# Performance work log

Hardware: AMD Instinct MI355X
Metric: run time of the kernel (lower is better)

The kernel has to match this reference:

```python
import jax, jax.numpy as jnp
import numpy as np
import itertools

F = 3          # num_sparse_features
C = 256        # num_categories
D = 64         # embedding_dim
H = 1024       # hidden_units
ND = 13        # num_dense_features
B = 16384      # batch
COMBOS = [c for r in range(2, F + 1) for c in itertools.combinations(range(F), r)]
WIDE_DIM = C * F + sum(C ** len(c) for c in COMBOS) + ND
DEEP_IN = F * D + ND


def setup_inputs() -> dict:
    key = jax.random.key(0)
    ks = jax.random.split(key, 12)
    sparse_inputs = jax.random.randint(ks[0], (B, F), 0, C, dtype=jnp.int32)
    dense_inputs = jax.random.normal(ks[1], (B, ND), dtype=jnp.float32)
    wide_w = jax.random.normal(ks[2], (WIDE_DIM,), dtype=jnp.float32) * 0.01
    wide_b = jax.random.normal(ks[3], (1,), dtype=jnp.float32) * 0.01
    emb = jax.random.normal(ks[4], (F, C, D), dtype=jnp.float32) * 0.05
    W1 = jax.random.normal(ks[5], (H, DEEP_IN), dtype=jnp.float32) / np.sqrt(DEEP_IN).astype(np.float32)
    b1 = jnp.zeros((H,), jnp.float32)
    W2 = jax.random.normal(ks[6], (H, H), dtype=jnp.float32) / np.sqrt(H).astype(np.float32)
    b2 = jnp.zeros((H,), jnp.float32)
    W3 = jax.random.normal(ks[7], (1, H), dtype=jnp.float32) / np.sqrt(H).astype(np.float32)
    b3 = jnp.zeros((1,), jnp.float32)
    return {"sparse_inputs": sparse_inputs, "dense_inputs": dense_inputs,
            "wide_w": wide_w, "wide_b": wide_b, "emb": emb,
            "W1": W1, "b1": b1, "W2": W2, "b2": b2, "W3": W3, "b3": b3}


def reference(sparse_inputs, dense_inputs, wide_w, wide_b, emb, W1, b1, W2, b2, W3, b3):
    # Wide path: one_hot(x) @ W.T  ==  gather of W columns at the hot indices.
    wide = wide_b[0]  # scalar, broadcasts to [B]
    for i in range(F):  # per-feature one-hot block, width C each
        wide = wide + wide_w[i * C + sparse_inputs[:, i]]
    off = F * C
    for combo in COMBOS:  # cross-feature one-hot blocks, width C**len(combo)
        cross = sparse_inputs[:, combo[0]]
        for j in combo[1:]:
            # faithful to source: multiplies by num_sparse_features (F), not C
            cross = cross * F + sparse_inputs[:, j]
        wide = wide + wide_w[off + cross]
        off += C ** len(combo)
    wide = wide + dense_inputs @ wide_w[off:off + ND]  # dense tail of wide linear
    wide = wide[:, None]  # [B, 1]

    # Deep path: per-feature embedding lookup -> concat -> 3-layer MLP
    embedded = jnp.concatenate([emb[i][sparse_inputs[:, i]] for i in range(F)], axis=1)  # [B, F*D]
    deep_x = jnp.concatenate([embedded, dense_inputs], axis=1)  # [B, DEEP_IN]
    h = jax.nn.relu(deep_x @ W1.T + b1)
    h = jax.nn.relu(h @ W2.T + b2)
    deep = h @ W3.T + b3  # [B, 1]

    return jax.nn.sigmoid(wide + deep)
```

## Files before the change

kernel.cpp:

```cpp
#include <hip/hip_runtime.h>
#include <stdint.h>


#define BATCH 16384
#define HDIM 1024
#define K1 224
#define DEEP_IN 205

typedef short bf16x8 __attribute__((ext_vector_type(8)));
typedef float f32x4 __attribute__((ext_vector_type(4)));
typedef uint16_t u16x8 __attribute__((ext_vector_type(8)));
typedef uint16_t u16x4 __attribute__((ext_vector_type(4)));

__device__ __forceinline__ uint16_t f2bf(float f) {
    uint32_t x;
    __builtin_memcpy(&x, &f, 4);
    uint32_t r = (x + 0x7fffu + ((x >> 16) & 1u)) >> 16;
    return (uint16_t)r;
}

__device__ __forceinline__ void async_ld16(const uint16_t* g, uint16_t* l) {
    __builtin_amdgcn_global_load_lds(
        (const __attribute__((address_space(1))) uint32_t*)g,
        (__attribute__((address_space(3))) uint32_t*)l, 16, 0, 0);
}

__global__ __launch_bounds__(256) void prep_kernel(
    const int* __restrict__ sp, const float* __restrict__ dense,
    const float* __restrict__ emb, const float* __restrict__ W1,
    uint16_t* __restrict__ dx, uint16_t* __restrict__ W1b)
{
    const int bid = blockIdx.x;
    if (bid < 1792) {
        int idx = bid * 256 + threadIdx.x;
        int b = idx / 28, c0 = (idx - b * 28) * 8;
        u16x8 o;
        if (c0 < 192) {
            int f = c0 >> 6, cc = c0 & 63;
            int s = sp[b * 3 + f];
            const float* e = emb + (size_t)(((f << 8) + s) * 64 + cc);
            float4 v0 = *(const float4*)e;
            float4 v1 = *(const float4*)(e + 4);
            o[0] = f2bf(v0.x); o[1] = f2bf(v0.y); o[2] = f2bf(v0.z); o[3] = f2bf(v0.w);
            o[4] = f2bf(v1.x); o[5] = f2bf(v1.y); o[6] = f2bf(v1.z); o[7] = f2bf(v1.w);
        } else {
#pragma unroll
            for (int t = 0; t < 8; t++) {
                int c = c0 + t;
                o[t] = (c < DEEP_IN) ? f2bf(dense[b * 13 + (c - 192)])
                                     : (uint16_t)0;
            }
        }
        *(u16x8*)(dx + (size_t)b * K1 + c0) = o;
    } else {
        int idx = (bid - 1792) * 256 + threadIdx.x;
        int n = idx / 28, c0 = (idx - n * 28) * 8;
        u16x8 o;
#pragma unroll
        for (int t = 0; t < 8; t++) {
            int c = c0 + t;
            o[t] = (c < DEEP_IN) ? f2bf(W1[n * DEEP_IN + c]) : (uint16_t)0;
        }
        *(u16x8*)(W1b + (size_t)n * K1 + c0) = o;
    }
}

#define GEMM_CORE(A_, B_, K_)                                                  \
    const int lane = tid & 63;                                                 \
    const int wave = tid >> 6;                                                 \
    const int wm = wave >> 2;                                                  \
    const int wn = wave & 3;                                                   \
    const int xcd = id & 7;                                                    \
    const int slot = id >> 3;                                                  \
    const int mbX = (M >> 7) >> 3;                                             \
    const int by = xcd * mbX + (slot >> 2);                                    \
    const int bx = slot & 3;                                                   \
    const int bm = by * 128;                                                   \
    const int bn = bx * 256;                                                   \
    const int rl = lane & 15, q = lane >> 4;                                   \
    f32x4 acc[4][4];                                                           \
    _Pragma("unroll") for (int i = 0; i < 4; i++)                              \
        _Pragma("unroll") for (int j = 0; j < 4; j++) acc[i][j] = (f32x4)0.f;  \
    const int cc0 = 2 * wave, cc1 = 2 * wave + 1;                              \
    const uint16_t* aS = A_ + (size_t)(bm + wave * 16 + rl) * K_ + q * 8;      \
    const uint16_t* bS0 = B_ + (size_t)(bn + (cc0 >> 2) * 64 + 4 * rl + (cc0 & 3)) * K_ + q * 8; \
    const uint16_t* bS1 = B_ + (size_t)(bn + (cc1 >> 2) * 64 + 4 * rl + (cc1 & 3)) * K_ + q * 8; \
    const int dA = wave * 512, dB0 = cc0 * 512, dB1 = cc1 * 512;               \
    async_ld16(aS, &Al[0][dA]);                                                \
    async_ld16(bS0, &Bl[0][dB0]);                                              \
    async_ld16(bS1, &Bl[0][dB1]);                                              \
    asm volatile("s_waitcnt vmcnt(0)" ::: "memory");                           \
    __syncthreads();                                                           \
    int p = 0;                                                                 \
    for (int k0 = 32; k0 < K_; k0 += 32) {                                     \
        async_ld16(aS + k0, &Al[p ^ 1][dA]);                                   \
        async_ld16(bS0 + k0, &Bl[p ^ 1][dB0]);                                 \
        async_ld16(bS1 + k0, &Bl[p ^ 1][dB1]);                                 \
        bf16x8 af[4], bfr[4];                                                  \
        _Pragma("unroll") for (int i = 0; i < 4; i++)                          \
            af[i] = *(const bf16x8*)&Al[p][(wm * 4 + i) * 512 + lane * 8];     \
        _Pragma("unroll") for (int j = 0; j < 4; j++)                          \
            bfr[j] = *(const bf16x8*)&Bl[p][(wn * 4 + j) * 512 + lane * 8];    \
        _Pragma("unroll") for (int i = 0; i < 4; i++)                          \
            _Pragma("unroll") for (int j = 0; j < 4; j++)                      \
                acc[i][j] = __builtin_amdgcn_mfma_f32_16x16x32_bf16(           \
                    af[i], bfr[j], acc[i][j], 0, 0, 0);                        \
        asm volatile("s_waitcnt vmcnt(0)" ::: "memory");                       \
        __syncthreads();                                                       \
        p ^= 1;                                                                \
    }                                                                          \
    {                                                                          \
        bf16x8 af[4], bfr[4];                                                  \
        _Pragma("unroll") for (int i = 0; i < 4; i++)                          \
            af[i] = *(const bf16x8*)&Al[p][(wm * 4 + i) * 512 + lane * 8];     \
        _Pragma("unroll") for (int j = 0; j < 4; j++)                          \
            bfr[j] = *(const bf16x8*)&Bl[p][(wn * 4 + j) * 512 + lane * 8];    \
        _Pragma("unroll") for (int i = 0; i < 4; i++)                          \
            _Pragma("unroll") for (int j = 0; j < 4; j++)                      \
                acc[i][j] = __builtin_amdgcn_mfma_f32_16x16x32_bf16(           \
                    af[i], bfr[j], acc[i][j], 0, 0, 0);                        \
    }

__global__ __launch_bounds__(512, 4) void gemm_relu(
    const uint16_t* __restrict__ A, const uint16_t* __restrict__ Bw,
    const float* __restrict__ bias, uint16_t* __restrict__ C,
    const float* __restrict__ W2, uint16_t* __restrict__ W2b,
    const int* __restrict__ sp, const float* __restrict__ dense,
    const float* __restrict__ ww, const float* __restrict__ wb,
    const float* __restrict__ b3, float* __restrict__ wide,
    int M, int N, int K)
{
    const int id = blockIdx.x;
    const int tid = threadIdx.x;

    if (id >= 512) {
        if (id < 768) {
            int k = (id - 512) * 512 + tid;
            const float* src = W2 + (size_t)k * 8;
            float4 v0 = *(const float4*)src;
            float4 v1 = *(const float4*)(src + 4);
            u16x8 o;
            o[0] = f2bf(v0.x); o[1] = f2bf(v0.y); o[2] = f2bf(v0.z); o[3] = f2bf(v0.w);
            o[4] = f2bf(v1.x); o[5] = f2bf(v1.y); o[6] = f2bf(v1.z); o[7] = f2bf(v1.w);
            *(u16x8*)(W2b + (size_t)k * 8) = o;
        } else {
            int b = (id - 768) * 512 + tid;
            int s0 = sp[b * 3], s1 = sp[b * 3 + 1], s2 = sp[b * 3 + 2];
            float w = wb[0] + b3[0];
            w += ww[s0] + ww[256 + s1] + ww[512 + s2];
            w += ww[768    + s0 * 3 + s1];
            w += ww[66304  + s0 * 3 + s2];
            w += ww[131840 + s1 * 3 + s2];
            w += ww[197376 + (s0 * 3 + s1) * 3 + s2];
            const float* wd = ww + 16974592;
            float acc2 = 0.f;
#pragma unroll
            for (int j = 0; j < 13; j++) acc2 += dense[b * 13 + j] * wd[j];
            wide[b] = w + acc2;
        }
        return;
    }

    __shared__ __align__(16) uint16_t Al[2][4096];
    __shared__ __align__(16) uint16_t Bl[2][8192];
    GEMM_CORE(A, Bw, K)

    float bv[4];
#pragma unroll
    for (int j = 0; j < 4; j++) bv[j] = bias[bn + wn * 64 + 4 * rl + j];
#pragma unroll
    for (int i = 0; i < 4; i++) {
#pragma unroll
        for (int r = 0; r < 4; r++) {
            int m = bm + wm * 64 + i * 16 + q * 4 + r;
            u16x4 o;
#pragma unroll
            for (int j = 0; j < 4; j++)
                o[j] = f2bf(fmaxf(acc[i][j][r] + bv[j], 0.f));
            *(u16x4*)&C[(size_t)m * N + bn + wn * 64 + 4 * rl] = o;
        }
    }
}

#define BAR8() do { asm volatile("" ::: "memory");                             \
    __builtin_amdgcn_s_barrier();                                              \
    asm volatile("" ::: "memory"); } while (0)
#define VM4() asm volatile("s_waitcnt vmcnt(4)" ::: "memory")

#define STG8(grow, regoff, h, kt) do {                                         \
    const uint16_t* g_ = (grow) + (size_t)((h) * 128) * (size_t)K + (kt);      \
    async_ld16(g_, &lds[(regoff) + (h) * 8192 + wave * 512]);                  \
    async_ld16(g_ + (size_t)64 * (size_t)K,                                    \
               &lds[(regoff) + (h) * 8192 + 4096 + wave * 512]);               \
} while (0)

#define LDA8(base, msub) do {                                                  \
    _Pragma("unroll") for (int mt = 0; mt < 4; mt++) {                         \
        int ro_ = (base) + ((msub) * 64 + mt * 16) * 64;                       \
        af[mt][0] = *(const bf16x8*)&lds[ro_ + kc0];                           \
        af[mt][1] = *(const bf16x8*)&lds[ro_ + kc1];                           \
    } } while (0)

#define LDB8(dst, base, nsub) do {                                             \
    _Pragma("unroll") for (int nt = 0; nt < 2; nt++) {                         \
        int ro_ = (base) + ((nsub) * 32 + nt * 16) * 64;                       \
        dst[nt][0] = *(const bf16x8*)&lds[ro_ + kc0];                          \
        dst[nt][1] = *(const bf16x8*)&lds[ro_ + kc1];                          \
    } } while (0)

#define MM8(msub, nsub, BF) do {                                               \
    __builtin_amdgcn_s_setprio(1);                                             \
    _Pragma("unroll") for (int mt = 0; mt < 4; mt++)                           \
    _Pragma("unroll") for (int nt = 0; nt < 2; nt++) {                         \
        acc[(msub)*4+mt][(nsub)*2+nt] = __builtin_amdgcn_mfma_f32_16x16x32_bf16( \
            af[mt][0], BF[nt][0], acc[(msub)*4+mt][(nsub)*2+nt], 0, 0, 0);     \
        acc[(msub)*4+mt][(nsub)*2+nt] = __builtin_amdgcn_mfma_f32_16x16x32_bf16( \
            af[mt][1], BF[nt][1], acc[(msub)*4+mt][(nsub)*2+nt], 0, 0, 0);     \
    }                                                                          \
    __builtin_amdgcn_s_setprio(0); } while (0)

__global__ __launch_bounds__(512, 2) void gemm_fused8(
    const uint16_t* __restrict__ A, const uint16_t* __restrict__ Bw,
    const float* __restrict__ bias, const float* __restrict__ W3,
    float* __restrict__ outacc, int M, int N, int K)
{
    __shared__ __align__(16) uint16_t lds[65536];
    const int tid = threadIdx.x;
    const int lane = tid & 63, wave = tid >> 6;
    const int wm = wave >> 2, wn = wave & 3;
    const int id = blockIdx.x;
    const int wg = (id & 7) * 32 + (id >> 3);
    const int by = wg >> 2, bx = wg & 3;
    const int bm = by * 256, bn = bx * 256;

    const int lam = lane & 15, lad = lane >> 4;
    const int sw = (lane & 7) << 4;
    const int kc0 = ((lad * 16) ^ sw) >> 1;
    const int kc1 = ((64 + lad * 16) ^ sw) >> 1;
    const int aBE = wm * 8192 + lam * 64;
    const int aBO = aBE + 16384;
    const int bBE = 32768 + (wn >> 1) * 8192 + ((wn & 1) * 64 + lam) * 64;
    const int bBO = bBE + 16384;

    const int trow = tid >> 3;
    const int csel = ((tid & 7) ^ (trow & 7)) << 3;
    const uint16_t* aRow = A + (size_t)(bm + trow) * K + csel;
    const uint16_t* bRow = Bw + (size_t)(bn + trow) * K + csel;

    f32x4 acc[8][4];
#pragma unroll
    for (int i = 0; i < 8; i++)
#pragma unroll
        for (int j = 0; j < 4; j++) acc[i][j] = (f32x4)0.f;
    bf16x8 af[4][2], bf0[2][2], bf1[2][2];

    const int NT = K >> 6;
    const int NI = K >> 7;

    STG8(aRow, 0, 0, 0);     STG8(aRow, 0, 1, 0);
    STG8(bRow, 32768, 0, 0); STG8(bRow, 32768, 1, 0);
    STG8(bRow, 49152, 0, 64); STG8(bRow, 49152, 1, 64);
    VM4();
    BAR8();

    for (int it = 0; it < NI; ++it) {
        const int k1 = (2 * it + 1) * 64;
        const int t2 = 2 * it + 2, t3 = 2 * it + 3;
        const int k2 = (t2 < NT ? t2 : 0) * 64;
        const int k3 = (t3 < NT ? t3 : 0) * 64;
        LDA8(aBE, 0); LDB8(bf0, bBE, 0); STG8(aRow, 16384, 0, k1);
        BAR8(); MM8(0, 0, bf0); BAR8();
        LDB8(bf1, bBE, 1); STG8(aRow, 16384, 1, k1);
        BAR8(); MM8(0, 1, bf1); BAR8();
        LDA8(aBE, 1); STG8(bRow, 32768, 0, k2);
        BAR8(); MM8(1, 1, bf1); BAR8();
        STG8(bRow, 32768, 1, k2);
        BAR8(); MM8(1, 0, bf0); VM4(); BAR8();
        LDA8(aBO, 0); LDB8(bf0, bBO, 0); STG8(aRow, 0, 0, k2);
        BAR8(); MM8(0, 0, bf0); BAR8();
        LDB8(bf1, bBO, 1); STG8(aRow, 0, 1, k2);
        BAR8(); MM8(0, 1, bf1); BAR8();
        LDA8(aBO, 1); STG8(bRow, 49152, 0, k3);
        BAR8(); MM8(1, 1, bf1); BAR8();
        STG8(bRow, 49152, 1, k3);
        BAR8(); MM8(1, 0, bf0); VM4(); BAR8();
    }

    float bv[4], w3v[4];
#pragma unroll
    for (int jn = 0; jn < 4; jn++) {
        int n = bn + wn * 64 + jn * 16 + lam;
        bv[jn] = bias[n];
        w3v[jn] = W3[n];
    }
#pragma unroll
    for (int im = 0; im < 8; im++) {
#pragma unroll
        for (int r = 0; r < 4; r++) {
            float pt = 0.f;
#pragma unroll
            for (int jn = 0; jn < 4; jn++)
                pt += fmaxf(acc[im][jn][r] + bv[jn], 0.f) * w3v[jn];
            pt += __shfl_xor(pt, 1);
            pt += __shfl_xor(pt, 2);
            pt += __shfl_xor(pt, 4);
            pt += __shfl_xor(pt, 8);
            if (lam == 0) {
                int m = bm + wm * 128 + im * 16 + lad * 4 + r;
                atomicAdd(&outacc[m], pt);
            }
        }
    }
}

__global__ __launch_bounds__(256) void sigmoid_kernel(
    const float* __restrict__ outacc, float* __restrict__ out)
{
    int b = blockIdx.x * 256 + threadIdx.x;
    out[b] = 1.f / (1.f + __expf(-outacc[b]));
}

extern "C" void kernel_launch(void* const* d_in, const int* in_sizes, int n_in,
                              void* d_out, int out_size, void* d_ws, size_t ws_size,
                              hipStream_t stream) {
    const int*   sp    = (const int*)d_in[0];
    const float* dense = (const float*)d_in[1];
    const float* ww    = (const float*)d_in[2];
    const float* wb    = (const float*)d_in[3];
    const float* emb   = (const float*)d_in[4];
    const float* W1    = (const float*)d_in[5];
    const float* b1    = (const float*)d_in[6];
    const float* W2    = (const float*)d_in[7];
    const float* b2    = (const float*)d_in[8];
    const float* W3    = (const float*)d_in[9];
    const float* b3    = (const float*)d_in[10];
    float* out = (float*)d_out;

    char* ws = (char*)d_ws;
    float*    wide = (float*)ws;
    uint16_t* dxp  = (uint16_t*)(ws + 65536);
    uint16_t* W1b  = (uint16_t*)(ws + 7405568);
    uint16_t* W2b  = (uint16_t*)(ws + 7864320);
    uint16_t* h1   = (uint16_t*)(ws + 9961472);

    prep_kernel<<<1904, 256, 0, stream>>>(sp, dense, emb, W1, dxp, W1b);
    gemm_relu<<<800, 512, 0, stream>>>(
        dxp, W1b, b1, h1, W2, W2b, sp, dense, ww, wb, b3, wide,
        BATCH, HDIM, K1);
    gemm_fused8<<<(BATCH / 256) * (HDIM / 256), 512, 0, stream>>>(
        h1, W2b, b2, W3, wide, BATCH, HDIM, HDIM);
    sigmoid_kernel<<<BATCH / 256, 256, 0, stream>>>(wide, out);
}
```

Baseline: 162.5 us.

## Pad layer-1 K to 256 and reuse the 256x256 pipelined GEMM for layer 1

```diff
diff --git a/kernel.cpp b/kernel.cpp
--- a/kernel.cpp
+++ b/kernel.cpp
@@ -4,7 +4,7 @@
 
 #define BATCH 16384
 #define HDIM 1024
-#define K1 224
+#define K1 256
 #define DEEP_IN 205
 
 typedef short bf16x8 __attribute__((ext_vector_type(8)));
@@ -28,12 +28,16 @@
 __global__ __launch_bounds__(256) void prep_kernel(
     const int* __restrict__ sp, const float* __restrict__ dense,
     const float* __restrict__ emb, const float* __restrict__ W1,
-    uint16_t* __restrict__ dx, uint16_t* __restrict__ W1b)
+    const float* __restrict__ W2, const float* __restrict__ ww,
+    const float* __restrict__ wb, const float* __restrict__ b3,
+    uint16_t* __restrict__ dx, uint16_t* __restrict__ W1b,
+    uint16_t* __restrict__ W2b, float* __restrict__ wide)
 {
     const int bid = blockIdx.x;
-    if (bid < 1792) {
-        int idx = bid * 256 + threadIdx.x;
-        int b = idx / 28, c0 = (idx - b * 28) * 8;
+    const int tid = threadIdx.x;
+    if (bid < 2048) {
+        int idx = bid * 256 + tid;
+        int b = idx >> 5, c0 = (idx & 31) * 8;
         u16x8 o;
         if (c0 < 192) {
             int f = c0 >> 6, cc = c0 & 63;
@@ -52,9 +56,9 @@
             }
         }
         *(u16x8*)(dx + (size_t)b * K1 + c0) = o;
-    } else {
-        int idx = (bid - 1792) * 256 + threadIdx.x;
-        int n = idx / 28, c0 = (idx - n * 28) * 8;
+    } else if (bid < 2176) {
+        int idx = (bid - 2048) * 256 + tid;
+        int n = idx >> 5, c0 = (idx & 31) * 8;
         u16x8 o;
 #pragma unroll
         for (int t = 0; t < 8; t++) {
@@ -62,123 +66,29 @@
             o[t] = (c < DEEP_IN) ? f2bf(W1[n * DEEP_IN + c]) : (uint16_t)0;
         }
         *(u16x8*)(W1b + (size_t)n * K1 + c0) = o;
-    }
-}
-
-#define GEMM_CORE(A_, B_, K_)                                                  \
-    const int lane = tid & 63;                                                 \
-    const int wave = tid >> 6;                                                 \
-    const int wm = wave >> 2;                                                  \
-    const int wn = wave & 3;                                                   \
-    const int xcd = id & 7;                                                    \
-    const int slot = id >> 3;                                                  \
-    const int mbX = (M >> 7) >> 3;                                             \
-    const int by = xcd * mbX + (slot >> 2);                                    \
-    const int bx = slot & 3;                                                   \
-    const int bm = by * 128;                                                   \
-    const int bn = bx * 256;                                                   \
-    const int rl = lane & 15, q = lane >> 4;                                   \
-    f32x4 acc[4][4];                                                           \
-    _Pragma("unroll") for (int i = 0; i < 4; i++)                              \
-        _Pragma("unroll") for (int j = 0; j < 4; j++) acc[i][j] = (f32x4)0.f;  \
-    const int cc0 = 2 * wave, cc1 = 2 * wave + 1;                              \
-    const uint16_t* aS = A_ + (size_t)(bm + wave * 16 + rl) * K_ + q * 8;      \
-    const uint16_t* bS0 = B_ + (size_t)(bn + (cc0 >> 2) * 64 + 4 * rl + (cc0 & 3)) * K_ + q * 8; \
-    const uint16_t* bS1 = B_ + (size_t)(bn + (cc1 >> 2) * 64 + 4 * rl + (cc1 & 3)) * K_ + q * 8; \
-    const int dA = wave * 512, dB0 = cc0 * 512, dB1 = cc1 * 512;               \
-    async_ld16(aS, &Al[0][dA]);                                                \
-    async_ld16(bS0, &Bl[0][dB0]);                                              \
-    async_ld16(bS1, &Bl[0][dB1]);                                              \
-    asm volatile("s_waitcnt vmcnt(0)" ::: "memory");                           \
-    __syncthreads();                                                           \
-    int p = 0;                                                                 \
-    for (int k0 = 32; k0 < K_; k0 += 32) {                                     \
-        async_ld16(aS + k0, &Al[p ^ 1][dA]);                                   \
-        async_ld16(bS0 + k0, &Bl[p ^ 1][dB0]);                                 \
-        async_ld16(bS1 + k0, &Bl[p ^ 1][dB1]);                                 \
-        bf16x8 af[4], bfr[4];                                                  \
-        _Pragma("unroll") for (int i = 0; i < 4; i++)                          \
-            af[i] = *(const bf16x8*)&Al[p][(wm * 4 + i) * 512 + lane * 8];     \
-        _Pragma("unroll") for (int j = 0; j < 4; j++)                          \
-            bfr[j] = *(const bf16x8*)&Bl[p][(wn * 4 + j) * 512 + lane * 8];    \
-        _Pragma("unroll") for (int i = 0; i < 4; i++)                          \
-            _Pragma("unroll") for (int j = 0; j < 4; j++)                      \
-                acc[i][j] = __builtin_amdgcn_mfma_f32_16x16x32_bf16(           \
-                    af[i], bfr[j], acc[i][j], 0, 0, 0);                        \
-        asm volatile("s_waitcnt vmcnt(0)" ::: "memory");                       \
-        __syncthreads();                                                       \
-        p ^= 1;                                                                \
-    }                                                                          \
-    {                                                                          \
-        bf16x8 af[4], bfr[4];                                                  \
-        _Pragma("unroll") for (int i = 0; i < 4; i++)                          \
-            af[i] = *(const bf16x8*)&Al[p][(wm * 4 + i) * 512 + lane * 8];     \
-        _Pragma("unroll") for (int j = 0; j < 4; j++)                          \
-            bfr[j] = *(const bf16x8*)&Bl[p][(wn * 4 + j) * 512 + lane * 8];    \
-        _Pragma("unroll") for (int i = 0; i < 4; i++)                          \
-            _Pragma("unroll") for (int j = 0; j < 4; j++)                      \
-                acc[i][j] = __builtin_amdgcn_mfma_f32_16x16x32_bf16(           \
-                    af[i], bfr[j], acc[i][j], 0, 0, 0);                        \
-    }
-
-__global__ __launch_bounds__(512, 4) void gemm_relu(
-    const uint16_t* __restrict__ A, const uint16_t* __restrict__ Bw,
-    const float* __restrict__ bias, uint16_t* __restrict__ C,
-    const float* __restrict__ W2, uint16_t* __restrict__ W2b,
-    const int* __restrict__ sp, const float* __restrict__ dense,
-    const float* __restrict__ ww, const float* __restrict__ wb,
-    const float* __restrict__ b3, float* __restrict__ wide,
-    int M, int N, int K)
-{
-    const int id = blockIdx.x;
-    const int tid = threadIdx.x;
-
-    if (id >= 512) {
-        if (id < 768) {
-            int k = (id - 512) * 512 + tid;
-            const float* src = W2 + (size_t)k * 8;
-            float4 v0 = *(const float4*)src;
-            float4 v1 = *(const float4*)(src + 4);
-            u16x8 o;
-            o[0] = f2bf(v0.x); o[1] = f2bf(v0.y); o[2] = f2bf(v0.z); o[3] = f2bf(v0.w);
-            o[4] = f2bf(v1.x); o[5] = f2bf(v1.y); o[6] = f2bf(v1.z); o[7] = f2bf(v1.w);
-            *(u16x8*)(W2b + (size_t)k * 8) = o;
-        } else {
-            int b = (id - 768) * 512 + tid;
-            int s0 = sp[b * 3], s1 = sp[b * 3 + 1], s2 = sp[b * 3 + 2];
-            float w = wb[0] + b3[0];
-            w += ww[s0] + ww[256 + s1] + ww[512 + s2];
-            w += ww[768    + s0 * 3 + s1];
-            w += ww[66304  + s0 * 3 + s2];
-            w += ww[131840 + s1 * 3 + s2];
-            w += ww[197376 + (s0 * 3 + s1) * 3 + s2];
-            const float* wd = ww + 16974592;
-            float acc2 = 0.f;
-#pragma unroll
-            for (int j = 0; j < 13; j++) acc2 += dense[b * 13 + j] * wd[j];
-            wide[b] = w + acc2;
-        }
-        return;
-    }
-
-    __shared__ __align__(16) uint16_t Al[2][4096];
-    __shared__ __align__(16) uint16_t Bl[2][8192];
-    GEMM_CORE(A, Bw, K)
-
-    float bv[4];
-#pragma unroll
-    for (int j = 0; j < 4; j++) bv[j] = bias[bn + wn * 64 + 4 * rl + j];
-#pragma unroll
-    for (int i = 0; i < 4; i++) {
-#pragma unroll
-        for (int r = 0; r < 4; r++) {
-            int m = bm + wm * 64 + i * 16 + q * 4 + r;
-            u16x4 o;
-#pragma unroll
-            for (int j = 0; j < 4; j++)
-                o[j] = f2bf(fmaxf(acc[i][j][r] + bv[j], 0.f));
-            *(u16x4*)&C[(size_t)m * N + bn + wn * 64 + 4 * rl] = o;
-        }
+    } else if (bid < 2688) {
+        int k = (bid - 2176) * 256 + tid;
+        const float* src = W2 + (size_t)k * 8;
+        float4 v0 = *(const float4*)src;
+        float4 v1 = *(const float4*)(src + 4);
+        u16x8 o;
+        o[0] = f2bf(v0.x); o[1] = f2bf(v0.y); o[2] = f2bf(v0.z); o[3] = f2bf(v0.w);
+        o[4] = f2bf(v1.x); o[5] = f2bf(v1.y); o[6] = f2bf(v1.z); o[7] = f2bf(v1.w);
+        *(u16x8*)(W2b + (size_t)k * 8) = o;
+    } else {
+        int b = (bid - 2688) * 256 + tid;
+        int s0 = sp[b * 3], s1 = sp[b * 3 + 1], s2 = sp[b * 3 + 2];
+        float w = wb[0] + b3[0];
+        w += ww[s0] + ww[256 + s1] + ww[512 + s2];
+        w += ww[768    + s0 * 3 + s1];
+        w += ww[66304  + s0 * 3 + s2];
+        w += ww[131840 + s1 * 3 + s2];
+        w += ww[197376 + (s0 * 3 + s1) * 3 + s2];
+        const float* wd = ww + 16974592;
+        float acc2 = 0.f;
+#pragma unroll
+        for (int j = 0; j < 13; j++) acc2 += dense[b * 13 + j] * wd[j];
+        wide[b] = w + acc2;
     }
 }
 
@@ -219,72 +129,99 @@
     }                                                                          \
     __builtin_amdgcn_s_setprio(0); } while (0)
 
+#define GEMM8_DECLS()                                                          \
+    const int tid = threadIdx.x;                                               \
+    const int lane = tid & 63, wave = tid >> 6;                                \
+    const int wm = wave >> 2, wn = wave & 3;                                   \
+    const int id = blockIdx.x;                                                 \
+    const int wg = (id & 7) * 32 + (id >> 3);                                  \
+    const int by = wg >> 2, bx = wg & 3;                                       \
+    const int bm = by * 256, bn = bx * 256;                                    \
+    const int lam = lane & 15, lad = lane >> 4;                                \
+    const int sw = (lane & 7) << 4;                                            \
+    const int kc0 = ((lad * 16) ^ sw) >> 1;                                    \
+    const int kc1 = ((64 + lad * 16) ^ sw) >> 1;                               \
+    const int aBE = wm * 8192 + lam * 64;                                      \
+    const int aBO = aBE + 16384;                                               \
+    const int bBE = 32768 + (wn >> 1) * 8192 + ((wn & 1) * 64 + lam) * 64;     \
+    const int bBO = bBE + 16384;                                               \
+    const int trow = tid >> 3;                                                 \
+    const int csel = ((tid & 7) ^ (trow & 7)) << 3;
+
+#define GEMM8_MAIN()                                                           \
+    f32x4 acc[8][4];                                                           \
+    _Pragma("unroll") for (int i = 0; i < 8; i++)                              \
+        _Pragma("unroll") for (int j = 0; j < 4; j++) acc[i][j] = (f32x4)0.f;  \
+    bf16x8 af[4][2], bf0[2][2], bf1[2][2];                                     \
+    const int NT = K >> 6;                                                     \
+    const int NI = K >> 7;                                                     \
+    STG8(aRow, 0, 0, 0);     STG8(aRow, 0, 1, 0);                              \
+    STG8(bRow, 32768, 0, 0); STG8(bRow, 32768, 1, 0);                          \
+    STG8(bRow, 49152, 0, 64); STG8(bRow, 49152, 1, 64);                        \
+    VM4();                                                                     \
+    BAR8();                                                                    \
+    for (int it = 0; it < NI; ++it) {                                          \
+        const int k1 = (2 * it + 1) * 64;                                      \
+        const int t2 = 2 * it + 2, t3 = 2 * it + 3;                            \
+        const int k2 = (t2 < NT ? t2 : 0) * 64;                                \
+        const int k3 = (t3 < NT ? t3 : 0) * 64;                                \
+        LDA8(aBE, 0); LDB8(bf0, bBE, 0); STG8(aRow, 16384, 0, k1);             \
+        BAR8(); MM8(0, 0, bf0); BAR8();                                        \
+        LDB8(bf1, bBE, 1); STG8(aRow, 16384, 1, k1);                           \
+        BAR8(); MM8(0, 1, bf1); BAR8();                                        \
+        LDA8(aBE, 1); STG8(bRow, 32768, 0, k2);                                \
+        BAR8(); MM8(1, 1, bf1); BAR8();                                        \
+        STG8(bRow, 32768, 1, k2);                                              \
+        BAR8(); MM8(1, 0, bf0); VM4(); BAR8();                                 \
+        LDA8(aBO, 0); LDB8(bf0, bBO, 0); STG8(aRow, 0, 0, k2);                 \
+        BAR8(); MM8(0, 0, bf0); BAR8();                                        \
+        LDB8(bf1, bBO, 1); STG8(aRow, 0, 1, k2);                               \
+        BAR8(); MM8(0, 1, bf1); BAR8();                                        \
+        LDA8(aBO, 1); STG8(bRow, 49152, 0, k3);                                \
+        BAR8(); MM8(1, 1, bf1); BAR8();                                        \
+        STG8(bRow, 49152, 1, k3);                                              \
+        BAR8(); MM8(1, 0, bf0); VM4(); BAR8();                                 \
+    }
+
+__global__ __launch_bounds__(512, 2) void gemm1_8(
+    const uint16_t* __restrict__ A, const uint16_t* __restrict__ Bw,
+    const float* __restrict__ bias, uint16_t* __restrict__ C,
+    int M, int N, int K)
+{
+    __shared__ __align__(16) uint16_t lds[65536];
+    GEMM8_DECLS()
+    const uint16_t* aRow = A + (size_t)(bm + trow) * K + csel;
+    const int prow = 4 * (trow & 15) + (trow >> 4);
+    const uint16_t* bRow = Bw + (size_t)(bn + prow) * K + csel;
+    GEMM8_MAIN()
+
+    float bv[4];
+#pragma unroll
+    for (int jn = 0; jn < 4; jn++) bv[jn] = bias[bn + wn * 64 + 4 * lam + jn];
+#pragma unroll
+    for (int im = 0; im < 8; im++) {
+#pragma unroll
+        for (int r = 0; r < 4; r++) {
+            int m = bm + wm * 128 + im * 16 + lad * 4 + r;
+            u16x4 o;
+#pragma unroll
+            for (int jn = 0; jn < 4; jn++)
+                o[jn] = f2bf(fmaxf(acc[im][jn][r] + bv[jn], 0.f));
+            *(u16x4*)&C[(size_t)m * N + bn + wn * 64 + 4 * lam] = o;
+        }
+    }
+}
+
 __global__ __launch_bounds__(512, 2) void gemm_fused8(
     const uint16_t* __restrict__ A, const uint16_t* __restrict__ Bw,
     const float* __restrict__ bias, const float* __restrict__ W3,
     float* __restrict__ outacc, int M, int N, int K)
 {
     __shared__ __align__(16) uint16_t lds[65536];
-    const int tid = threadIdx.x;
-    const int lane = tid & 63, wave = tid >> 6;
-    const int wm = wave >> 2, wn = wave & 3;
-    const int id = blockIdx.x;
-    const int wg = (id & 7) * 32 + (id >> 3);
-    const int by = wg >> 2, bx = wg & 3;
-    const int bm = by * 256, bn = bx * 256;
-
-    const int lam = lane & 15, lad = lane >> 4;
-    const int sw = (lane & 7) << 4;
-    const int kc0 = ((lad * 16) ^ sw) >> 1;
-    const int kc1 = ((64 + lad * 16) ^ sw) >> 1;
-    const int aBE = wm * 8192 + lam * 64;
-    const int aBO = aBE + 16384;
-    const int bBE = 32768 + (wn >> 1) * 8192 + ((wn & 1) * 64 + lam) * 64;
-    const int bBO = bBE + 16384;
-
-    const int trow = tid >> 3;
-    const int csel = ((tid & 7) ^ (trow & 7)) << 3;
+    GEMM8_DECLS()
     const uint16_t* aRow = A + (size_t)(bm + trow) * K + csel;
     const uint16_t* bRow = Bw + (size_t)(bn + trow) * K + csel;
-
-    f32x4 acc[8][4];
-#pragma unroll
-    for (int i = 0; i < 8; i++)
-#pragma unroll
-        for (int j = 0; j < 4; j++) acc[i][j] = (f32x4)0.f;
-    bf16x8 af[4][2], bf0[2][2], bf1[2][2];
-
-    const int NT = K >> 6;
-    const int NI = K >> 7;
-
-    STG8(aRow, 0, 0, 0);     STG8(aRow, 0, 1, 0);
-    STG8(bRow, 32768, 0, 0); STG8(bRow, 32768, 1, 0);
-    STG8(bRow, 49152, 0, 64); STG8(bRow, 49152, 1, 64);
-    VM4();
-    BAR8();
-
-    for (int it = 0; it < NI; ++it) {
-        const int k1 = (2 * it + 1) * 64;
-        const int t2 = 2 * it + 2, t3 = 2 * it + 3;
-        const int k2 = (t2 < NT ? t2 : 0) * 64;
-        const int k3 = (t3 < NT ? t3 : 0) * 64;
-        LDA8(aBE, 0); LDB8(bf0, bBE, 0); STG8(aRow, 16384, 0, k1);
-        BAR8(); MM8(0, 0, bf0); BAR8();
-        LDB8(bf1, bBE, 1); STG8(aRow, 16384, 1, k1);
-        BAR8(); MM8(0, 1, bf1); BAR8();
-        LDA8(aBE, 1); STG8(bRow, 32768, 0, k2);
-        BAR8(); MM8(1, 1, bf1); BAR8();
-        STG8(bRow, 32768, 1, k2);
-        BAR8(); MM8(1, 0, bf0); VM4(); BAR8();
-        LDA8(aBO, 0); LDB8(bf0, bBO, 0); STG8(aRow, 0, 0, k2);
-        BAR8(); MM8(0, 0, bf0); BAR8();
-        LDB8(bf1, bBO, 1); STG8(aRow, 0, 1, k2);
-        BAR8(); MM8(0, 1, bf1); BAR8();
-        LDA8(aBO, 1); STG8(bRow, 49152, 0, k3);
-        BAR8(); MM8(1, 1, bf1); BAR8();
-        STG8(bRow, 49152, 1, k3);
-        BAR8(); MM8(1, 0, bf0); VM4(); BAR8();
-    }
+    GEMM8_MAIN()
 
     float bv[4], w3v[4];
 #pragma unroll
@@ -339,15 +276,15 @@
     char* ws = (char*)d_ws;
     float*    wide = (float*)ws;
     uint16_t* dxp  = (uint16_t*)(ws + 65536);
-    uint16_t* W1b  = (uint16_t*)(ws + 7405568);
-    uint16_t* W2b  = (uint16_t*)(ws + 7864320);
-    uint16_t* h1   = (uint16_t*)(ws + 9961472);
-
-    prep_kernel<<<1904, 256, 0, stream>>>(sp, dense, emb, W1, dxp, W1b);
-    gemm_relu<<<800, 512, 0, stream>>>(
-        dxp, W1b, b1, h1, W2, W2b, sp, dense, ww, wb, b3, wide,
-        BATCH, HDIM, K1);
-    gemm_fused8<<<(BATCH / 256) * (HDIM / 256), 512, 0, stream>>>(
+    uint16_t* W1b  = (uint16_t*)(ws + 8454144);
+    uint16_t* W2b  = (uint16_t*)(ws + 8978432);
+    uint16_t* h1   = (uint16_t*)(ws + 11075584);
+
+    prep_kernel<<<2752, 256, 0, stream>>>(
+        sp, dense, emb, W1, W2, ww, wb, b3, dxp, W1b, W2b, wide);
+    gemm1_8<<<256, 512, 0, stream>>>(
+        dxp, W1b, b1, h1, BATCH, HDIM, K1);
+    gemm_fused8<<<256, 512, 0, stream>>>(
         h1, W2b, b2, W3, wide, BATCH, HDIM, HDIM);
     sigmoid_kernel<<<BATCH / 256, 256, 0, stream>>>(wide, out);
 }
```

After: 160.7 us. No clear change (-1.1%).
